# Optimization experiments

Hardware: AMD Instinct MI355X
Metric: run time of the kernel (lower is better)

Reference implementation:

```python
import jax, jax.numpy as jnp
import numpy as np

COORD = 5.0   # self.coord
NOOBJ = 0.5   # self.noobj
B = 32768
S = 7.0       # grid size, hard-coded as /7 in the original


def setup_inputs() -> dict:
    key = jax.random.key(0)
    k1, k2, k3 = jax.random.split(key, 3)
    # min 0.01 keeps sqrt(wh) and its gradient finite (original takes sqrt of raw preds)
    output = jax.random.uniform(k1, (B, 7, 7, 30), dtype=jnp.float32, minval=0.01, maxval=1.0)
    target = jax.random.uniform(k2, (B, 7, 7, 30), dtype=jnp.float32, minval=0.01, maxval=1.0)
    obj = (jax.random.uniform(k3, (B, 7, 7)) < 0.15).astype(jnp.float32)
    target = target.at[..., 4].set(obj).at[..., 9].set(obj)
    return {"output": output, "target": target}


def reference(output, target):
    dt = output.dtype
    w_obj = (target[..., 4] > 0).astype(dt)      # (B,7,7) object-cell mask
    w_no = 1.0 - w_obj                            # no-object cells

    out_b = output[..., :10].reshape(output.shape[0], 7, 7, 2, 5)
    tgt_b = target[..., :10].reshape(target.shape[0], 7, 7, 2, 5)
    out_cls = output[..., 10:]
    tgt_cls = target[..., 10:]

    # class MSE (sum) over object cells
    class_loss = jnp.sum(w_obj[..., None] * (out_cls - tgt_cls) ** 2)
    accurate_num = jnp.sum(w_obj * (jnp.argmax(out_cls, -1) == jnp.argmax(tgt_cls, -1)).astype(dt))

    # box corners: xy/7 -+ 0.5*wh (as in the original)
    o_xy, o_wh = out_b[..., :2] / S, out_b[..., 2:4]
    o_lt, o_rb = o_xy - 0.5 * o_wh, o_xy + 0.5 * o_wh          # (B,7,7,2,2)
    t_box = tgt_b[..., 0, :]                                    # target box 0 (as in loop: target_boxes[i])
    t_xy, t_wh = t_box[..., :2] / S, t_box[..., 2:4]
    t_lt = (t_xy - 0.5 * t_wh)[..., None, :]                    # (B,7,7,1,2)
    t_rb = (t_xy + 0.5 * t_wh)[..., None, :]

    # torchvision.ops.box_iou: inter / (area1 + area2 - inter), widths clamped at 0
    inter_wh = jnp.clip(jnp.minimum(o_rb, t_rb) - jnp.maximum(o_lt, t_lt), 0.0)
    inter = inter_wh[..., 0] * inter_wh[..., 1]                 # (B,7,7,2)
    area_o = (o_rb - o_lt)[..., 0] * (o_rb - o_lt)[..., 1]
    area_t = (t_rb - t_lt)[..., 0] * (t_rb - t_lt)[..., 1]
    iou = inter / (area_o + area_t - inter)                     # (B,7,7,2)

    resp = jnp.argmax(iou, -1)                                  # responsible box index
    max_iou = jnp.max(iou, -1)
    left = jax.nn.one_hot(resp, 2, dtype=dt)                    # (B,7,7,2)

    out_sel = jnp.sum(left[..., None] * out_b, axis=-2)         # responsible predicted box
    tgt_sel = jnp.sum(left[..., None] * tgt_b, axis=-2)         # target box at same slot
    out_ab = jnp.sum((1.0 - left)[..., None] * out_b, axis=-2)  # abandoned predicted box

    coord_loss = jnp.sum(w_obj * (
        jnp.sum((out_sel[..., :2] - tgt_sel[..., :2]) ** 2, -1)
        + jnp.sum((jnp.sqrt(out_sel[..., 2:4]) - jnp.sqrt(tgt_sel[..., 2:4])) ** 2, -1)))
    conf_loss = jnp.sum(w_obj * (out_sel[..., 4] - max_iou) ** 2)
    abandon_loss = jnp.sum(w_obj * out_ab[..., 4] ** 2)         # box_iou target is 0 at abandoned slot
    noobj_loss = jnp.sum(w_no[..., None] * (out_b[..., 4] - tgt_b[..., 4]) ** 2)

    total = COORD * coord_loss + conf_loss + NOOBJ * (noobj_loss + abandon_loss) + class_loss
    sum_iou = jnp.sum(w_obj * max_iou)
    return total, sum_iou, accurate_num
```

## Files before the change

### kernel.cpp

```cpp
#include <hip/hip_runtime.h>
#include <stdint.h>

#define S_INV (1.0f / 7.0f)
#define COORD_W 5.0f
#define NOOBJ_W 0.5f

#define SLICE_FLOATS 3840
#define WAVES_PER_BLOCK 4

typedef const __attribute__((address_space(1))) void* gp1_t;
typedef __attribute__((address_space(3))) void* lp3_t;

__device__ __forceinline__ void stage_chunk(const float* __restrict__ outp,
                                            const float* __restrict__ tgtp,
                                            float* dst, int m, int lane)
{
    const size_t cb = (size_t)m * (64 * 120);
#pragma unroll
    for (int j = 0; j < 15; ++j) {
        const int off = j * 1024 + lane * 16;
        const char* src = (off < 7680)
            ? (const char*)outp + cb + off
            : (const char*)tgtp + cb + (off - 7680);
        __builtin_amdgcn_global_load_lds((gp1_t)src, (lp3_t)(dst + j * 256),
                                         16, 0, 0);
    }
}

__global__ __launch_bounds__(256) void yolo_loss_kernel(
    const float* __restrict__ outp, const float* __restrict__ tgtp,
    float* __restrict__ ws, int nchunks, int nwaves)
{
    __shared__ float lds[WAVES_PER_BLOCK * 2 * SLICE_FLOATS];

    const int wave = threadIdx.x >> 6;
    const int lane = threadIdx.x & 63;
    const int gwave = blockIdx.x * WAVES_PER_BLOCK + wave;

    float* bufA = lds + wave * 2 * SLICE_FLOATS;
    float* bufB = bufA + SLICE_FLOATS;

    float acc_total = 0.f, acc_iou = 0.f, acc_acc = 0.f;

    if (gwave < nchunks) stage_chunk(outp, tgtp, bufA, gwave, lane);
    int cur = 0;

    for (int m = gwave; m < nchunks; m += nwaves) {
        const bool has_next = (m + nwaves) < nchunks;
        float* bnext = cur ? bufA : bufB;
        float* bcur  = cur ? bufB : bufA;

        if (has_next) {
            stage_chunk(outp, tgtp, bnext, m + nwaves, lane);
            asm volatile("s_waitcnt vmcnt(15)" ::: "memory");
        } else {
            asm volatile("s_waitcnt vmcnt(0)" ::: "memory");
        }
        __builtin_amdgcn_sched_barrier(0);

        const float* oc = bcur + lane * 30;
        const float* tc = bcur + 1920 + lane * 30;
        float ov[30], tv[30];
#pragma unroll
        for (int i = 0; i < 15; ++i) {
            float2 a = *reinterpret_cast<const float2*>(oc + 2 * i);
            float2 b = *reinterpret_cast<const float2*>(tc + 2 * i);
            ov[2 * i] = a.x; ov[2 * i + 1] = a.y;
            tv[2 * i] = b.x; tv[2 * i + 1] = b.y;
        }

        float w_obj = (tv[4] > 0.f) ? 1.f : 0.f;
        float w_no = 1.f - w_obj;

        float cls = 0.f;
        float omax = ov[10]; int oarg = 0;
        float tmax = tv[10]; int targ = 0;
#pragma unroll
        for (int c = 0; c < 20; ++c) {
            float d = ov[10 + c] - tv[10 + c];
            cls += d * d;
            if (ov[10 + c] > omax) { omax = ov[10 + c]; oarg = c; }
            if (tv[10 + c] > tmax) { tmax = tv[10 + c]; targ = c; }
        }

        float t_x = tv[0] * S_INV, t_y = tv[1] * S_INV;
        float t_w = tv[2], t_h = tv[3];
        float t_l = t_x - 0.5f * t_w, t_r = t_x + 0.5f * t_w;
        float t_t = t_y - 0.5f * t_h, t_b = t_y + 0.5f * t_h;
        float area_t = t_w * t_h;

        float iou0, iou1;
        {
            float x = ov[0] * S_INV, y = ov[1] * S_INV;
            float w = ov[2], h = ov[3];
            float l = x - 0.5f * w, r = x + 0.5f * w;
            float tt = y - 0.5f * h, bb = y + 0.5f * h;
            float iw = fmaxf(fminf(r, t_r) - fmaxf(l, t_l), 0.f);
            float ih = fmaxf(fminf(bb, t_b) - fmaxf(tt, t_t), 0.f);
            float inter = iw * ih;
            iou0 = inter / (w * h + area_t - inter);
        }
        {
            float x = ov[5] * S_INV, y = ov[6] * S_INV;
            float w = ov[7], h = ov[8];
            float l = x - 0.5f * w, r = x + 0.5f * w;
            float tt = y - 0.5f * h, bb = y + 0.5f * h;
            float iw = fmaxf(fminf(r, t_r) - fmaxf(l, t_l), 0.f);
            float ih = fmaxf(fminf(bb, t_b) - fmaxf(tt, t_t), 0.f);
            float inter = iw * ih;
            iou1 = inter / (w * h + area_t - inter);
        }

        bool r1 = (iou1 > iou0);
        float max_iou = r1 ? iou1 : iou0;

        float os0 = r1 ? ov[5] : ov[0];
        float os1 = r1 ? ov[6] : ov[1];
        float os2 = r1 ? ov[7] : ov[2];
        float os3 = r1 ? ov[8] : ov[3];
        float os4 = r1 ? ov[9] : ov[4];
        float ts0 = r1 ? tv[5] : tv[0];
        float ts1 = r1 ? tv[6] : tv[1];
        float ts2 = r1 ? tv[7] : tv[2];
        float ts3 = r1 ? tv[8] : tv[3];
        float oa4 = r1 ? ov[4] : ov[9];

        float d0 = os0 - ts0, d1 = os1 - ts1;
        float d2 = sqrtf(os2) - sqrtf(ts2);
        float d3 = sqrtf(os3) - sqrtf(ts3);
        float coord = d0 * d0 + d1 * d1 + d2 * d2 + d3 * d3;

        float dc = os4 - max_iou;
        float conf = dc * dc;
        float aband = oa4 * oa4;
        float n0 = ov[4] - tv[4], n1 = ov[9] - tv[9];
        float noobj = n0 * n0 + n1 * n1;

        float cell_total = w_obj * (COORD_W * coord + conf + NOOBJ_W * aband + cls)
                         + NOOBJ_W * w_no * noobj;

        acc_total += cell_total;
        acc_iou   += w_obj * max_iou;
        acc_acc   += w_obj * ((oarg == targ) ? 1.f : 0.f);

        __builtin_amdgcn_sched_barrier(0);
        cur ^= 1;
    }

#pragma unroll
    for (int off = 32; off > 0; off >>= 1) {
        acc_total += __shfl_down(acc_total, off);
        acc_iou   += __shfl_down(acc_iou, off);
        acc_acc   += __shfl_down(acc_acc, off);
    }
    if (lane == 0) {
        ws[gwave]              = acc_total;
        ws[nwaves + gwave]     = acc_iou;
        ws[2 * nwaves + gwave] = acc_acc;
    }
}

__global__ __launch_bounds__(256) void yolo_reduce_kernel(
    const float* __restrict__ ws, float* __restrict__ out, int nwaves)
{
    float t0 = 0.f, t1 = 0.f, t2 = 0.f;
    for (int i = threadIdx.x; i < nwaves; i += blockDim.x) {
        t0 += ws[i];
        t1 += ws[nwaves + i];
        t2 += ws[2 * nwaves + i];
    }
#pragma unroll
    for (int off = 32; off > 0; off >>= 1) {
        t0 += __shfl_down(t0, off);
        t1 += __shfl_down(t1, off);
        t2 += __shfl_down(t2, off);
    }
    __shared__ float s[3][4];
    int wave = threadIdx.x >> 6;
    int lane = threadIdx.x & 63;
    if (lane == 0) { s[0][wave] = t0; s[1][wave] = t1; s[2][wave] = t2; }
    __syncthreads();
    if (threadIdx.x == 0) {
        float a0 = 0.f, a1 = 0.f, a2 = 0.f;
#pragma unroll
        for (int w = 0; w < 4; ++w) { a0 += s[0][w]; a1 += s[1][w]; a2 += s[2][w]; }
        out[0] = a0;
        out[1] = a1;
        out[2] = a2;
    }
}

extern "C" void kernel_launch(void* const* d_in, const int* in_sizes, int n_in,
                              void* d_out, int out_size, void* d_ws, size_t ws_size,
                              hipStream_t stream) {
    const float* outp = (const float*)d_in[0];
    const float* tgtp = (const float*)d_in[1];
    float* ws = (float*)d_ws;
    float* o = (float*)d_out;

    const int ncells  = in_sizes[0] / 30;
    const int nchunks = ncells / 64;
    const int blocks  = 256;
    const int nwaves  = blocks * WAVES_PER_BLOCK;

    yolo_loss_kernel<<<blocks, 256, 0, stream>>>(outp, tgtp, ws, nchunks, nwaves);
    yolo_reduce_kernel<<<1, 256, 0, stream>>>(ws, o, nwaves);
}
```

Measured before the change: 73.55 us.

## Use single-wave blocks with 32-cell chunks and many more waves

Switches from 256-thread blocks of four waves over 64-cell chunks to 2560 one-wave blocks that each stream 32-cell chunks through a double-buffered LDS slice. Only half the lanes compute per chunk, and the staging adds a 4-byte tail load to cover the non-1KB-aligned chunk size. The goal is more concurrent waves and more memory requests in flight for this bandwidth-bound reduction. The cost is idle lanes during compute, more partial sums for the final reduce, and smaller per-wave transfers.

```diff
diff --git a/kernel.cpp b/kernel.cpp
--- a/kernel.cpp
+++ b/kernel.cpp
@@ -5,8 +5,9 @@
 #define COORD_W 5.0f
 #define NOOBJ_W 0.5f
 
-#define SLICE_FLOATS 3840
-#define WAVES_PER_BLOCK 4
+#define CHUNK_CELLS 32
+#define BUF_FLOATS 1920
+#define CHUNK_BYTES (CHUNK_CELLS * 120)
 
 typedef const __attribute__((address_space(1))) void* gp1_t;
 typedef __attribute__((address_space(3))) void* lp3_t;
@@ -15,30 +16,38 @@
                                             const float* __restrict__ tgtp,
                                             float* dst, int m, int lane)
 {
-    const size_t cb = (size_t)m * (64 * 120);
-#pragma unroll
-    for (int j = 0; j < 15; ++j) {
+    const size_t cb = (size_t)m * CHUNK_BYTES;
+#pragma unroll
+    for (int j = 0; j < 7; ++j) {
         const int off = j * 1024 + lane * 16;
-        const char* src = (off < 7680)
+        const char* src = (off < 3840)
             ? (const char*)outp + cb + off
-            : (const char*)tgtp + cb + (off - 7680);
-        __builtin_amdgcn_global_load_lds((gp1_t)src, (lp3_t)(dst + j * 256),
+            : (const char*)tgtp + cb + (off - 3840);
+        __builtin_amdgcn_global_load_lds((gp1_t)src,
+                                         (lp3_t)((char*)dst + j * 1024),
                                          16, 0, 0);
     }
-}
-
-__global__ __launch_bounds__(256) void yolo_loss_kernel(
+#pragma unroll
+    for (int j = 0; j < 2; ++j) {
+        const int off = 7168 + j * 256 + lane * 4;
+        const char* src = (const char*)tgtp + cb + (off - 3840);
+        __builtin_amdgcn_global_load_lds((gp1_t)src,
+                                         (lp3_t)((char*)dst + 7168 + j * 256),
+                                         4, 0, 0);
+    }
+}
+
+__global__ __launch_bounds__(64) void yolo_loss_kernel(
     const float* __restrict__ outp, const float* __restrict__ tgtp,
     float* __restrict__ ws, int nchunks, int nwaves)
 {
-    __shared__ float lds[WAVES_PER_BLOCK * 2 * SLICE_FLOATS];
-
-    const int wave = threadIdx.x >> 6;
-    const int lane = threadIdx.x & 63;
-    const int gwave = blockIdx.x * WAVES_PER_BLOCK + wave;
-
-    float* bufA = lds + wave * 2 * SLICE_FLOATS;
-    float* bufB = bufA + SLICE_FLOATS;
+    __shared__ float lds[2 * BUF_FLOATS];
+
+    const int lane = threadIdx.x;
+    const int gwave = blockIdx.x;
+
+    float* bufA = lds;
+    float* bufB = lds + BUF_FLOATS;
 
     float acc_total = 0.f, acc_iou = 0.f, acc_acc = 0.f;
 
@@ -52,96 +61,96 @@
 
         if (has_next) {
             stage_chunk(outp, tgtp, bnext, m + nwaves, lane);
-            asm volatile("s_waitcnt vmcnt(15)" ::: "memory");
+            asm volatile("s_waitcnt vmcnt(9)" ::: "memory");
         } else {
             asm volatile("s_waitcnt vmcnt(0)" ::: "memory");
         }
         __builtin_amdgcn_sched_barrier(0);
 
-        const float* oc = bcur + lane * 30;
-        const float* tc = bcur + 1920 + lane * 30;
-        float ov[30], tv[30];
-#pragma unroll
-        for (int i = 0; i < 15; ++i) {
-            float2 a = *reinterpret_cast<const float2*>(oc + 2 * i);
-            float2 b = *reinterpret_cast<const float2*>(tc + 2 * i);
-            ov[2 * i] = a.x; ov[2 * i + 1] = a.y;
-            tv[2 * i] = b.x; tv[2 * i + 1] = b.y;
+        if (lane < CHUNK_CELLS) {
+            const float* oc = bcur + lane * 30;
+            const float* tc = bcur + 960 + lane * 30;
+            float ov[30], tv[30];
+#pragma unroll
+            for (int i = 0; i < 15; ++i) {
+                float2 a = *reinterpret_cast<const float2*>(oc + 2 * i);
+                float2 b = *reinterpret_cast<const float2*>(tc + 2 * i);
+                ov[2 * i] = a.x; ov[2 * i + 1] = a.y;
+                tv[2 * i] = b.x; tv[2 * i + 1] = b.y;
+            }
+
+            float w_obj = (tv[4] > 0.f) ? 1.f : 0.f;
+            float w_no = 1.f - w_obj;
+
+            float cls = 0.f;
+            float omax = ov[10]; int oarg = 0;
+            float tmax = tv[10]; int targ = 0;
+#pragma unroll
+            for (int c = 0; c < 20; ++c) {
+                float d = ov[10 + c] - tv[10 + c];
+                cls += d * d;
+                if (ov[10 + c] > omax) { omax = ov[10 + c]; oarg = c; }
+                if (tv[10 + c] > tmax) { tmax = tv[10 + c]; targ = c; }
+            }
+
+            float t_x = tv[0] * S_INV, t_y = tv[1] * S_INV;
+            float t_w = tv[2], t_h = tv[3];
+            float t_l = t_x - 0.5f * t_w, t_r = t_x + 0.5f * t_w;
+            float t_t = t_y - 0.5f * t_h, t_b = t_y + 0.5f * t_h;
+            float area_t = t_w * t_h;
+
+            float iou0, iou1;
+            {
+                float x = ov[0] * S_INV, y = ov[1] * S_INV;
+                float w = ov[2], h = ov[3];
+                float l = x - 0.5f * w, r = x + 0.5f * w;
+                float tt = y - 0.5f * h, bb = y + 0.5f * h;
+                float iw = fmaxf(fminf(r, t_r) - fmaxf(l, t_l), 0.f);
+                float ih = fmaxf(fminf(bb, t_b) - fmaxf(tt, t_t), 0.f);
+                float inter = iw * ih;
+                iou0 = inter / (w * h + area_t - inter);
+            }
+            {
+                float x = ov[5] * S_INV, y = ov[6] * S_INV;
+                float w = ov[7], h = ov[8];
+                float l = x - 0.5f * w, r = x + 0.5f * w;
+                float tt = y - 0.5f * h, bb = y + 0.5f * h;
+                float iw = fmaxf(fminf(r, t_r) - fmaxf(l, t_l), 0.f);
+                float ih = fmaxf(fminf(bb, t_b) - fmaxf(tt, t_t), 0.f);
+                float inter = iw * ih;
+                iou1 = inter / (w * h + area_t - inter);
+            }
+
+            bool r1 = (iou1 > iou0);
+            float max_iou = r1 ? iou1 : iou0;
+
+            float os0 = r1 ? ov[5] : ov[0];
+            float os1 = r1 ? ov[6] : ov[1];
+            float os2 = r1 ? ov[7] : ov[2];
+            float os3 = r1 ? ov[8] : ov[3];
+            float os4 = r1 ? ov[9] : ov[4];
+            float ts0 = r1 ? tv[5] : tv[0];
+            float ts1 = r1 ? tv[6] : tv[1];
+            float ts2 = r1 ? tv[7] : tv[2];
+            float ts3 = r1 ? tv[8] : tv[3];
+            float oa4 = r1 ? ov[4] : ov[9];
+
+            float d0 = os0 - ts0, d1 = os1 - ts1;
+            float d2 = sqrtf(os2) - sqrtf(ts2);
+            float d3 = sqrtf(os3) - sqrtf(ts3);
+            float coord = d0 * d0 + d1 * d1 + d2 * d2 + d3 * d3;
+
+            float dc = os4 - max_iou;
+            float conf = dc * dc;
+            float aband = oa4 * oa4;
+            float n0 = ov[4] - tv[4], n1 = ov[9] - tv[9];
+            float noobj = n0 * n0 + n1 * n1;
+
+            acc_total += w_obj * (COORD_W * coord + conf + NOOBJ_W * aband + cls)
+                       + NOOBJ_W * w_no * noobj;
+            acc_iou   += w_obj * max_iou;
+            acc_acc   += w_obj * ((oarg == targ) ? 1.f : 0.f);
         }
-
-        float w_obj = (tv[4] > 0.f) ? 1.f : 0.f;
-        float w_no = 1.f - w_obj;
-
-        float cls = 0.f;
-        float omax = ov[10]; int oarg = 0;
-        float tmax = tv[10]; int targ = 0;
-#pragma unroll
-        for (int c = 0; c < 20; ++c) {
-            float d = ov[10 + c] - tv[10 + c];
-            cls += d * d;
-            if (ov[10 + c] > omax) { omax = ov[10 + c]; oarg = c; }
-            if (tv[10 + c] > tmax) { tmax = tv[10 + c]; targ = c; }
-        }
-
-        float t_x = tv[0] * S_INV, t_y = tv[1] * S_INV;
-        float t_w = tv[2], t_h = tv[3];
-        float t_l = t_x - 0.5f * t_w, t_r = t_x + 0.5f * t_w;
-        float t_t = t_y - 0.5f * t_h, t_b = t_y + 0.5f * t_h;
-        float area_t = t_w * t_h;
-
-        float iou0, iou1;
-        {
-            float x = ov[0] * S_INV, y = ov[1] * S_INV;
-            float w = ov[2], h = ov[3];
-            float l = x - 0.5f * w, r = x + 0.5f * w;
-            float tt = y - 0.5f * h, bb = y + 0.5f * h;
-            float iw = fmaxf(fminf(r, t_r) - fmaxf(l, t_l), 0.f);
-            float ih = fmaxf(fminf(bb, t_b) - fmaxf(tt, t_t), 0.f);
-            float inter = iw * ih;
-            iou0 = inter / (w * h + area_t - inter);
-        }
-        {
-            float x = ov[5] * S_INV, y = ov[6] * S_INV;
-            float w = ov[7], h = ov[8];
-            float l = x - 0.5f * w, r = x + 0.5f * w;
-            float tt = y - 0.5f * h, bb = y + 0.5f * h;
-            float iw = fmaxf(fminf(r, t_r) - fmaxf(l, t_l), 0.f);
-            float ih = fmaxf(fminf(bb, t_b) - fmaxf(tt, t_t), 0.f);
-            float inter = iw * ih;
-            iou1 = inter / (w * h + area_t - inter);
-        }
-
-        bool r1 = (iou1 > iou0);
-        float max_iou = r1 ? iou1 : iou0;
-
-        float os0 = r1 ? ov[5] : ov[0];
-        float os1 = r1 ? ov[6] : ov[1];
-        float os2 = r1 ? ov[7] : ov[2];
-        float os3 = r1 ? ov[8] : ov[3];
-        float os4 = r1 ? ov[9] : ov[4];
-        float ts0 = r1 ? tv[5] : tv[0];
-        float ts1 = r1 ? tv[6] : tv[1];
-        float ts2 = r1 ? tv[7] : tv[2];
-        float ts3 = r1 ? tv[8] : tv[3];
-        float oa4 = r1 ? ov[4] : ov[9];
-
-        float d0 = os0 - ts0, d1 = os1 - ts1;
-        float d2 = sqrtf(os2) - sqrtf(ts2);
-        float d3 = sqrtf(os3) - sqrtf(ts3);
-        float coord = d0 * d0 + d1 * d1 + d2 * d2 + d3 * d3;
-
-        float dc = os4 - max_iou;
-        float conf = dc * dc;
-        float aband = oa4 * oa4;
-        float n0 = ov[4] - tv[4], n1 = ov[9] - tv[9];
-        float noobj = n0 * n0 + n1 * n1;
-
-        float cell_total = w_obj * (COORD_W * coord + conf + NOOBJ_W * aband + cls)
-                         + NOOBJ_W * w_no * noobj;
-
-        acc_total += cell_total;
-        acc_iou   += w_obj * max_iou;
-        acc_acc   += w_obj * ((oarg == targ) ? 1.f : 0.f);
 
         __builtin_amdgcn_sched_barrier(0);
         cur ^= 1;
@@ -199,10 +208,10 @@
     float* o = (float*)d_out;
 
     const int ncells  = in_sizes[0] / 30;
-    const int nchunks = ncells / 64;
-    const int blocks  = 256;
-    const int nwaves  = blocks * WAVES_PER_BLOCK;
-
-    yolo_loss_kernel<<<blocks, 256, 0, stream>>>(outp, tgtp, ws, nchunks, nwaves);
+    const int nchunks = ncells / CHUNK_CELLS;
+    const int blocks  = 2560;
+    const int nwaves  = blocks;
+
+    yolo_loss_kernel<<<blocks, 64, 0, stream>>>(outp, tgtp, ws, nchunks, nwaves);
     yolo_reduce_kernel<<<1, 256, 0, stream>>>(ws, o, nwaves);
 }
```

Result: slower. 79.24 us (+7.7%).

## Split staging per array across two waves with block barriers and larger chunks

Applied to the files above, without the earlier changes.

Restructures the staging so each 128-thread block handles 128-cell chunks. One wave streams the output array and the other streams the target array into shared double buffers, with s_barrier calls to synchronise the two waves. The intent is longer contiguous global reads per wave and more blocks in flight (640 instead of 256), so memory bandwidth is better used. In exchange it adds two block barriers per iteration and changes the occupancy and LDS footprint per block.

```diff
diff --git a/kernel.cpp b/kernel.cpp
--- a/kernel.cpp
+++ b/kernel.cpp
@@ -5,61 +5,62 @@
 #define COORD_W 5.0f
 #define NOOBJ_W 0.5f
 
-#define SLICE_FLOATS 3840
-#define WAVES_PER_BLOCK 4
+#define CHUNK_CELLS 128
+#define BUF_FLOATS 7680
+#define ARR_BYTES  15360
 
 typedef const __attribute__((address_space(1))) void* gp1_t;
 typedef __attribute__((address_space(3))) void* lp3_t;
 
-__device__ __forceinline__ void stage_chunk(const float* __restrict__ outp,
-                                            const float* __restrict__ tgtp,
-                                            float* dst, int m, int lane)
+__device__ __forceinline__ void stage_half(const float* __restrict__ arr,
+                                           size_t cb, float* buf,
+                                           int wave, int lane)
 {
-    const size_t cb = (size_t)m * (64 * 120);
+    char* dst = (char*)buf + wave * ARR_BYTES;
 #pragma unroll
     for (int j = 0; j < 15; ++j) {
-        const int off = j * 1024 + lane * 16;
-        const char* src = (off < 7680)
-            ? (const char*)outp + cb + off
-            : (const char*)tgtp + cb + (off - 7680);
-        __builtin_amdgcn_global_load_lds((gp1_t)src, (lp3_t)(dst + j * 256),
+        const char* src = (const char*)arr + cb + j * 1024 + lane * 16;
+        __builtin_amdgcn_global_load_lds((gp1_t)src, (lp3_t)(dst + j * 1024),
                                          16, 0, 0);
     }
 }
 
-__global__ __launch_bounds__(256) void yolo_loss_kernel(
+__global__ __launch_bounds__(128) void yolo_loss_kernel(
     const float* __restrict__ outp, const float* __restrict__ tgtp,
-    float* __restrict__ ws, int nchunks, int nwaves)
+    float* __restrict__ ws, int nchunks, int nblocks)
 {
-    __shared__ float lds[WAVES_PER_BLOCK * 2 * SLICE_FLOATS];
-
-    const int wave = threadIdx.x >> 6;
-    const int lane = threadIdx.x & 63;
-    const int gwave = blockIdx.x * WAVES_PER_BLOCK + wave;
-
-    float* bufA = lds + wave * 2 * SLICE_FLOATS;
-    float* bufB = bufA + SLICE_FLOATS;
+    __shared__ float lds[2 * BUF_FLOATS];
+
+    const int tid  = threadIdx.x;
+    const int wave = tid >> 6;
+    const int lane = tid & 63;
+
+    float* bufA = lds;
+    float* bufB = lds + BUF_FLOATS;
+    const float* myarr = wave ? tgtp : outp;
 
     float acc_total = 0.f, acc_iou = 0.f, acc_acc = 0.f;
 
-    if (gwave < nchunks) stage_chunk(outp, tgtp, bufA, gwave, lane);
+    stage_half(myarr, (size_t)blockIdx.x * ARR_BYTES, bufA, wave, lane);
     int cur = 0;
 
-    for (int m = gwave; m < nchunks; m += nwaves) {
-        const bool has_next = (m + nwaves) < nchunks;
+    for (int m = blockIdx.x; m < nchunks; m += nblocks) {
+        const bool has_next = (m + nblocks) < nchunks;
         float* bnext = cur ? bufA : bufB;
         float* bcur  = cur ? bufB : bufA;
 
         if (has_next) {
-            stage_chunk(outp, tgtp, bnext, m + nwaves, lane);
+            stage_half(myarr, (size_t)(m + nblocks) * ARR_BYTES, bnext, wave, lane);
             asm volatile("s_waitcnt vmcnt(15)" ::: "memory");
         } else {
             asm volatile("s_waitcnt vmcnt(0)" ::: "memory");
         }
         __builtin_amdgcn_sched_barrier(0);
-
-        const float* oc = bcur + lane * 30;
-        const float* tc = bcur + 1920 + lane * 30;
+        __builtin_amdgcn_s_barrier();
+        __builtin_amdgcn_sched_barrier(0);
+
+        const float* oc = bcur + tid * 30;
+        const float* tc = bcur + 3840 + tid * 30;
         float ov[30], tv[30];
 #pragma unroll
         for (int i = 0; i < 15; ++i) {
@@ -136,13 +137,13 @@
         float n0 = ov[4] - tv[4], n1 = ov[9] - tv[9];
         float noobj = n0 * n0 + n1 * n1;
 
-        float cell_total = w_obj * (COORD_W * coord + conf + NOOBJ_W * aband + cls)
-                         + NOOBJ_W * w_no * noobj;
-
-        acc_total += cell_total;
+        acc_total += w_obj * (COORD_W * coord + conf + NOOBJ_W * aband + cls)
+                   + NOOBJ_W * w_no * noobj;
         acc_iou   += w_obj * max_iou;
         acc_acc   += w_obj * ((oarg == targ) ? 1.f : 0.f);
 
+        __builtin_amdgcn_sched_barrier(0);
+        __builtin_amdgcn_s_barrier();
         __builtin_amdgcn_sched_barrier(0);
         cur ^= 1;
     }
@@ -153,10 +154,12 @@
         acc_iou   += __shfl_down(acc_iou, off);
         acc_acc   += __shfl_down(acc_acc, off);
     }
+    const int gwid = blockIdx.x * 2 + wave;
+    const int nwaves = nblocks * 2;
     if (lane == 0) {
-        ws[gwave]              = acc_total;
-        ws[nwaves + gwave]     = acc_iou;
-        ws[2 * nwaves + gwave] = acc_acc;
+        ws[gwid]              = acc_total;
+        ws[nwaves + gwid]     = acc_iou;
+        ws[2 * nwaves + gwid] = acc_acc;
     }
 }
 
@@ -199,10 +202,10 @@
     float* o = (float*)d_out;
 
     const int ncells  = in_sizes[0] / 30;
-    const int nchunks = ncells / 64;
-    const int blocks  = 256;
-    const int nwaves  = blocks * WAVES_PER_BLOCK;
-
-    yolo_loss_kernel<<<blocks, 256, 0, stream>>>(outp, tgtp, ws, nchunks, nwaves);
+    const int nchunks = ncells / CHUNK_CELLS;
+    const int blocks  = 640;
+    const int nwaves  = blocks * 2;
+
+    yolo_loss_kernel<<<blocks, 128, 0, stream>>>(outp, tgtp, ws, nchunks, blocks);
     yolo_reduce_kernel<<<1, 256, 0, stream>>>(ws, o, nwaves);
 }
```

New measurement: 96.09 us. 30.6% more time.
